# Optimization experiments

Hardware: AMD Instinct MI355X
Metric: run time of the kernel (lower is better)

Reference implementation:

```python
import jax, jax.numpy as jnp
import numpy as np

N_META, M_SUB = 64, 1024          # n meta-nodes, m nodes per sub-graph
D_IN, D_HID, D_OUT = 128, 128, 64
NUM_LAYERS_EXTRA, K = 2, 3        # total DSGraphGLayers = NUM_LAYERS_EXTRA + 1
N_EDGES = 1048576                 # ~avg degree 16 over 65536 nodes


def setup_inputs() -> dict:
    key = jax.random.key(0)
    ks = jax.random.split(key, 8)
    N = N_META * M_SUB
    x = jax.random.normal(ks[0], (N_META, M_SUB, D_IN), jnp.float32)
    sub_adj = jax.random.randint(ks[1], (2, N_EDGES), 0, N, dtype=jnp.int32)
    # dense binary meta-graph adjacency (n, n)
    adj = (jax.random.uniform(ks[2], (N_META, N_META)) < 0.1).astype(jnp.float32)
    L = NUM_LAYERS_EXTRA + 1
    scale = 1.0 / np.sqrt(D_HID).astype(np.float32)
    gcn_W = jax.random.normal(ks[3], (L, K + 1, D_HID, D_HID), jnp.float32) * scale
    gcn_b = jnp.zeros((L, K + 1, D_HID), jnp.float32)
    lin_W1 = jax.random.normal(ks[4], (D_HID, D_HID), jnp.float32) * scale
    lin_b1 = jnp.zeros((D_HID,), jnp.float32)
    lin_W2 = jax.random.normal(ks[5], (D_HID, D_OUT), jnp.float32) * scale
    lin_b2 = jnp.zeros((D_OUT,), jnp.float32)
    return dict(x=x, sub_adj=sub_adj, adj=adj, gcn_W=gcn_W, gcn_b=gcn_b,
                lin_W1=lin_W1, lin_b1=lin_b1, lin_W2=lin_W2, lin_b2=lin_b2)


def _gcn_conv(x, src, dst, dinv, W, b, N):
    norm = dinv[src] * dinv[dst]                      # [E+N]
    msg = (x @ W)[src] * norm[:, None]                # [E+N, d_out]
    return jax.ops.segment_sum(msg, dst, num_segments=N) + b


def reference(x, sub_adj, adj, gcn_W, gcn_b, lin_W1, lin_b1, lin_W2, lin_b2):
    n, m, d = x.shape
    N = n * m
    loops = jnp.arange(N, dtype=sub_adj.dtype)
    src = jnp.concatenate([sub_adj[0], loops])
    dst = jnp.concatenate([sub_adj[1], loops])
    deg = jax.ops.segment_sum(jnp.ones(src.shape, x.dtype), dst, num_segments=N)
    dinv = jnp.where(deg > 0, jax.lax.rsqrt(deg), jnp.zeros_like(deg))
    # precompute_adj: cached_adj = [adj, adj^2, ..., adj^K]; powers >= 2 detached in source
    cached = [adj]
    A = adj
    for _ in range(K - 1):
        A = jax.lax.stop_gradient(A @ adj)
        cached.append(A)
    for li in range(gcn_W.shape[0]):
        xf = x.reshape(N, -1)
        out = _gcn_conv(xf, src, dst, dinv, gcn_W[li, 0], gcn_b[li, 0], N)
        for i, Ai in enumerate(cached):
            # meta-graph mixing: x_i[n,m,d] = sum_j A_i[n,j] * x[j,m,d]
            xi = jnp.einsum('nj,jmd->nmd', Ai, x).reshape(N, -1)
            out = out + _gcn_conv(xi, src, dst, dinv, gcn_W[li, i + 1], gcn_b[li, i + 1], N)
        x = jax.nn.relu(out.reshape(n, m, -1))
    h = x.reshape(N, -1)
    h = jax.nn.relu(h @ lin_W1 + lin_b1)
    h = h @ lin_W2 + lin_b2
    return h.reshape(n, m, -1)
```

## Files before the change

### kernel.cpp

```cpp
#include <hip/hip_runtime.h>

#define NMETA 64
#define MSUB 1024
#define NNODES 65536
#define D 128
#define DOUT 64
#define NEDGES 1048576
#define COLS 131072
#define BCAP 5120

typedef __attribute__((ext_vector_type(8))) short bf8_t;
typedef __attribute__((ext_vector_type(4))) float f4_t;
typedef __attribute__((ext_vector_type(2))) float f2_t;

__device__ inline unsigned short bfr(float x) {
    unsigned u = __builtin_bit_cast(unsigned, x);
    u += 0x7fffu + ((u >> 16) & 1u);
    return (unsigned short)(u >> 16);
}
__device__ inline float b2f(unsigned short h) {
    return __builtin_bit_cast(float, (unsigned)h << 16);
}
__device__ inline f2_t up2(unsigned u) {
    f2_t r;
    r[0] = __builtin_bit_cast(float, u << 16);
    r[1] = __builtin_bit_cast(float, u & 0xffff0000u);
    return r;
}

__global__ __launch_bounds__(256) void k_bhist(const int* __restrict__ dst,
                                               int* __restrict__ whist) {
    __shared__ int c[256];
    int t = threadIdx.x, w = blockIdx.x;
    c[t] = 0;
    __syncthreads();
    const int* dp = dst + w * 4096;
    for (int k = 0; k < 16; ++k) atomicAdd(&c[dp[k * 256 + t] >> 8], 1);
    __syncthreads();
    whist[t * 256 + w] = c[t];
}

__global__ __launch_bounds__(256) void k_bscan(int* __restrict__ whist,
                                               int* __restrict__ bbase) {
    __shared__ int sh[256];
    int t = threadIdx.x;
    int run = 0;
    for (int w = 0; w < 256; ++w) {
        int v = whist[t * 256 + w];
        whist[t * 256 + w] = run;
        run += v;
    }
    sh[t] = run;
    __syncthreads();
    for (int d = 1; d < 256; d <<= 1) {
        int x = (t >= d) ? sh[t - d] : 0;
        __syncthreads();
        sh[t] += x;
        __syncthreads();
    }
    bbase[t] = sh[t] - run;
    if (t == 255) bbase[256] = NEDGES;
}

__global__ __launch_bounds__(256) void k_bscatter(const int* __restrict__ src,
                                                  const int* __restrict__ dst,
                                                  const int* __restrict__ bbase,
                                                  const int* __restrict__ whist,
                                                  unsigned* __restrict__ tmp) {
    __shared__ int cur[256];
    __shared__ int base[256];
    int t = threadIdx.x, w = blockIdx.x;
    cur[t] = 0;
    base[t] = bbase[t] + whist[t * 256 + w];
    __syncthreads();
    const int* dp = dst + w * 4096;
    const int* sp = src + w * 4096;
    for (int k = 0; k < 16; ++k) {
        int d = dp[k * 256 + t], s = sp[k * 256 + t];
        int b = d >> 8;
        int lr = atomicAdd(&cur[b], 1);
        tmp[base[b] + lr] = ((unsigned)(d & 255) << 16) | (unsigned)s;
    }
}

__global__ __launch_bounds__(256) void k_bcsr(const unsigned* __restrict__ tmp,
                                              const int* __restrict__ bbase,
                                              int* __restrict__ offs,
                                              float* __restrict__ dinv,
                                              unsigned short* __restrict__ csr16) {
    __shared__ unsigned pairs[BCAP];
    __shared__ unsigned short image[BCAP];
    __shared__ int cnt[256], cur[256], sh[256];
    int t = threadIdx.x, b = blockIdx.x;
    int base = bbase[b], n = bbase[b + 1] - base;
    for (int i = t; i < n; i += 256) pairs[i] = tmp[base + i];
    cnt[t] = 0;
    __syncthreads();
    for (int i = t; i < n; i += 256) atomicAdd(&cnt[pairs[i] >> 16], 1);
    __syncthreads();
    int c = cnt[t];
    sh[t] = c;
    __syncthreads();
    for (int d = 1; d < 256; d <<= 1) {
        int x = (t >= d) ? sh[t - d] : 0;
        __syncthreads();
        sh[t] += x;
        __syncthreads();
    }
    int excl = sh[t] - c;
    cur[t] = excl;
    offs[b * 256 + t] = base + excl;
    dinv[b * 256 + t] = rsqrtf((float)(c + 1));
    if (b == 255 && t == 255) offs[65536] = NEDGES;
    __syncthreads();
    for (int i = t; i < n; i += 256) {
        unsigned p = pairs[i];
        int pos = atomicAdd(&cur[p >> 16], 1);
        image[pos] = (unsigned short)(p & 0xffffu);
    }
    __syncthreads();
    {
        int s0 = excl, s1 = excl + c;
        for (int i = s0 + 1; i < s1; ++i) {
            unsigned short key = image[i];
            int j = i - 1;
            while (j >= s0 && image[j] > key) { image[j + 1] = image[j]; --j; }
            image[j + 1] = key;
        }
    }
    __syncthreads();
    for (int i = t; i < n; i += 256) csr16[base + i] = image[i];
}

__global__ __launch_bounds__(256) void k_setup(const float* __restrict__ A,
                                               unsigned short* __restrict__ Ab,
                                               const float* __restrict__ gcnW,
                                               const float* __restrict__ W1,
                                               const float* __restrict__ W2,
                                               unsigned short* __restrict__ Wt) {
    int blk = blockIdx.x, t = threadIdx.x;
    if (blk == 0) {
        __shared__ float As[4096];
        __shared__ float Bs[4096];
        for (int q = 0; q < 16; ++q) As[t + 256 * q] = A[t + 256 * q];
        __syncthreads();
        for (int q = 0; q < 16; ++q) {
            int idx = t + 256 * q;
            int n = idx >> 6, j = idx & 63;
            Ab[idx] = bfr(As[idx]);
            float acc = 0.f;
            for (int k = 0; k < 64; ++k) acc += As[n * 64 + k] * As[k * 64 + j];
            Bs[idx] = acc;
            Ab[4096 + idx] = bfr(acc);
        }
        __syncthreads();
        for (int q = 0; q < 16; ++q) {
            int idx = t + 256 * q;
            int n = idx >> 6, j = idx & 63;
            float acc = 0.f;
            for (int k = 0; k < 64; ++k) acc += Bs[n * 64 + k] * As[k * 64 + j];
            Ab[8192 + idx] = bfr(acc);
        }
    } else {
        int b2 = blk - 1;
        int m = b2 >> 6;
        int idx = (b2 & 63) * 256 + t;
        const float* src;
        int N = 128;
        if (m < 12)       src = gcnW + m * 16384;
        else if (m == 12) src = W1;
        else { src = W2; N = 64; if (idx >= 8192) return; }
        int n = idx >> 7, k = idx & 127;
        Wt[m * 16384 + idx] = bfr(src[k * N + n]);
    }
}

#define TS 130
template <bool INF32>
__global__ __launch_bounds__(256) void k_layer(const unsigned short* __restrict__ X,
                                               const float* __restrict__ Xf,
                                               const unsigned short* __restrict__ Ab,
                                               const unsigned short* __restrict__ Wt4,
                                               const float* __restrict__ dinv,
                                               unsigned short* __restrict__ Y) {
    __shared__ unsigned short LB[3 * 64 * TS];
    __shared__ float dsh[64];
    int t = threadIdx.x;
    int m = blockIdx.x;
    int wave = t >> 6, lane = t & 63;
    int l16 = lane & 15, kg = lane >> 4;
    int c0 = wave * 32;

    if (t < 64) dsh[t] = dinv[(long)t * MSUB + m];

#pragma unroll
    for (int it = 0; it < 4; ++it) {
        int slot = it * 256 + t;
        int row = slot >> 4, ch = slot & 15;
        if (INF32) {
            const float* xp = Xf + ((long)row * MSUB + m) * D + ch * 8;
            float4 va = *(const float4*)xp;
            float4 vb = *(const float4*)(xp + 4);
            uint4 pk;
            pk.x = ((unsigned)bfr(va.y) << 16) | bfr(va.x);
            pk.y = ((unsigned)bfr(va.w) << 16) | bfr(va.z);
            pk.z = ((unsigned)bfr(vb.y) << 16) | bfr(vb.x);
            pk.w = ((unsigned)bfr(vb.w) << 16) | bfr(vb.z);
            *(uint4*)&LB[row * 128 + ch * 8] = pk;
        } else {
            *(uint4*)&LB[row * 128 + ch * 8] =
                *(const uint4*)(X + ((long)row * MSUB + m) * D + ch * 8);
        }
    }
    __syncthreads();

    bf8_t xa[4][4];
#pragma unroll
    for (int mt = 0; mt < 4; ++mt)
#pragma unroll
        for (int kb = 0; kb < 4; ++kb)
            xa[mt][kb] = *(const bf8_t*)&LB[(mt * 16 + l16) * 128 + kb * 32 + kg * 8];
    __syncthreads();

    f4_t zero4 = {0.f, 0.f, 0.f, 0.f};

    f4_t accT0[4][2];
#pragma unroll
    for (int mt = 0; mt < 4; ++mt)
#pragma unroll
        for (int nt = 0; nt < 2; ++nt) accT0[mt][nt] = zero4;
#pragma unroll
    for (int kb = 0; kb < 4; ++kb)
#pragma unroll
        for (int nt = 0; nt < 2; ++nt) {
            bf8_t b = *(const bf8_t*)(Wt4 + (long)(c0 + nt * 16 + l16) * 128 +
                                      kb * 32 + kg * 8);
#pragma unroll
            for (int mt = 0; mt < 4; ++mt)
                accT0[mt][nt] = __builtin_amdgcn_mfma_f32_16x16x32_bf16(
                    xa[mt][kb], b, accT0[mt][nt], 0, 0, 0);
        }

#pragma unroll
    for (int z = 1; z < 4; ++z) {
        f4_t acc[4][2];
#pragma unroll
        for (int mt = 0; mt < 4; ++mt)
#pragma unroll
            for (int nt = 0; nt < 2; ++nt) acc[mt][nt] = zero4;
        const unsigned short* wp = Wt4 + z * 16384;
#pragma unroll
        for (int kb = 0; kb < 4; ++kb)
#pragma unroll
            for (int nt = 0; nt < 2; ++nt) {
                bf8_t b = *(const bf8_t*)(wp + (long)(c0 + nt * 16 + l16) * 128 +
                                          kb * 32 + kg * 8);
#pragma unroll
                for (int mt = 0; mt < 4; ++mt)
                    acc[mt][nt] = __builtin_amdgcn_mfma_f32_16x16x32_bf16(
                        xa[mt][kb], b, acc[mt][nt], 0, 0, 0);
            }
#pragma unroll
        for (int mt = 0; mt < 4; ++mt)
#pragma unroll
            for (int nt = 0; nt < 2; ++nt)
#pragma unroll
                for (int r = 0; r < 4; ++r)
                    LB[((z - 1) * 64 + mt * 16 + kg * 4 + r) * TS +
                       c0 + nt * 16 + l16] = bfr(acc[mt][nt][r]);
    }

    f4_t acc2[4][2];
#pragma unroll
    for (int mt = 0; mt < 4; ++mt)
#pragma unroll
        for (int nt = 0; nt < 2; ++nt) acc2[mt][nt] = zero4;
#pragma unroll
    for (int i = 0; i < 3; ++i)
#pragma unroll
        for (int kb = 0; kb < 2; ++kb) {
            bf8_t af[4];
#pragma unroll
            for (int mt = 0; mt < 4; ++mt)
                af[mt] = *(const bf8_t*)(Ab + i * 4096 + (mt * 16 + l16) * 64 +
                                         kb * 32 + kg * 8);
#pragma unroll
            for (int nt = 0; nt < 2; ++nt) {
                bf8_t b;
#pragma unroll
                for (int jj = 0; jj < 8; ++jj)
                    b[jj] = (short)LB[(i * 64 + kb * 32 + kg * 8 + jj) * TS +
                                      c0 + nt * 16 + l16];
#pragma unroll
                for (int mt = 0; mt < 4; ++mt)
                    acc2[mt][nt] = __builtin_amdgcn_mfma_f32_16x16x32_bf16(
                        af[mt], b, acc2[mt][nt], 0, 0, 0);
            }
        }

#pragma unroll
    for (int mt = 0; mt < 4; ++mt)
#pragma unroll
        for (int nt = 0; nt < 2; ++nt)
#pragma unroll
            for (int r = 0; r < 4; ++r) {
                int row = mt * 16 + kg * 4 + r;
                int col = c0 + nt * 16 + l16;
                float v = (acc2[mt][nt][r] + accT0[mt][nt][r]) * dsh[row];
                Y[((long)row * MSUB + m) * D + col] = bfr(v);
            }
}

__global__ __launch_bounds__(256) void k_prop(const unsigned short* __restrict__ Y,
                                              const int* __restrict__ offs,
                                              const unsigned short* __restrict__ csr,
                                              const float* __restrict__ dinv,
                                              const float* __restrict__ bias4,
                                              unsigned short* __restrict__ Xout) {
    int wid = threadIdx.x >> 6;
    int lane = threadIdx.x & 63;
    int q = lane >> 4;
    int l = lane & 15;
    int v = blockIdx.x * 4 + wid;
    const uint4* Y4 = (const uint4*)Y;
    int e0 = offs[v], e1 = offs[v + 1];
    f2_t acc2[4];
#pragma unroll
    for (int k = 0; k < 4; ++k) acc2[k] = (f2_t){0.f, 0.f};

    int e = e0 + q;
    for (; e + 4 < e1; e += 8) {
        int u0 = csr[e], u1 = csr[e + 4];
        uint4 y0 = Y4[(long)u0 * 16 + l];
        uint4 y1 = Y4[(long)u1 * 16 + l];
        acc2[0] += up2(y0.x) + up2(y1.x);
        acc2[1] += up2(y0.y) + up2(y1.y);
        acc2[2] += up2(y0.z) + up2(y1.z);
        acc2[3] += up2(y0.w) + up2(y1.w);
    }
    if (e < e1) {
        int u = csr[e];
        uint4 y = Y4[(long)u * 16 + l];
        acc2[0] += up2(y.x);
        acc2[1] += up2(y.y);
        acc2[2] += up2(y.z);
        acc2[3] += up2(y.w);
    }
    float acc[8];
#pragma unroll
    for (int k = 0; k < 4; ++k) { acc[2 * k] = acc2[k][0]; acc[2 * k + 1] = acc2[k][1]; }
#pragma unroll
    for (int k = 0; k < 8; ++k) {
        acc[k] += __shfl_xor(acc[k], 32, 64);
        acc[k] += __shfl_xor(acc[k], 16, 64);
    }
    if (q == 0) {
        float dv = dinv[v];
        uint4 s = Y4[(long)v * 16 + l];
        f2_t s2[4] = {up2(s.x), up2(s.y), up2(s.z), up2(s.w)};
        float bs[8];
#pragma unroll
        for (int k = 0; k < 8; ++k) bs[k] = 0.f;
#pragma unroll
        for (int p = 0; p < 4; ++p) {
            float4 blo = *(const float4*)(bias4 + p * 128 + l * 8);
            float4 bhi = *(const float4*)(bias4 + p * 128 + l * 8 + 4);
            bs[0] += blo.x; bs[1] += blo.y; bs[2] += blo.z; bs[3] += blo.w;
            bs[4] += bhi.x; bs[5] += bhi.y; bs[6] += bhi.z; bs[7] += bhi.w;
        }
        unsigned r[8];
#pragma unroll
        for (int k = 0; k < 8; ++k) {
            float sf = s2[k / 2][k % 2];
            r[k] = bfr(fmaxf(dv * (acc[k] + sf) + bs[k], 0.f));
        }
        uint4 pk;
        pk.x = (r[1] << 16) | r[0];
        pk.y = (r[3] << 16) | r[2];
        pk.z = (r[5] << 16) | r[4];
        pk.w = (r[7] << 16) | r[6];
        ((uint4*)Xout)[(long)v * 16 + l] = pk;
    }
}

#define HST 136
__global__ __launch_bounds__(256) void k_mlp(const unsigned short* __restrict__ X,
                                             const unsigned short* __restrict__ Wt,
                                             const float* __restrict__ b1,
                                             const float* __restrict__ b2,
                                             float* __restrict__ out) {
    __shared__ unsigned short H[128 * HST];
    int wave = threadIdx.x >> 6, lane = threadIdx.x & 63;
    int l16 = lane & 15, kg = lane >> 4;
    long row0 = (long)blockIdx.x * 128 + wave * 32;
    int hb = wave * 32 * HST;

    bf8_t a[2][4];
    const unsigned short* xp = X + row0 * 128 + kg * 8;
#pragma unroll
    for (int kb = 0; kb < 4; ++kb) {
        a[0][kb] = *(const bf8_t*)(xp + (long)l16 * 128 + kb * 32);
        a[1][kb] = *(const bf8_t*)(xp + (long)(l16 + 16) * 128 + kb * 32);
    }
    f4_t zero4 = {0.f, 0.f, 0.f, 0.f};
    f4_t acc[2][8];
#pragma unroll
    for (int mt = 0; mt < 2; ++mt)
#pragma unroll
        for (int nt = 0; nt < 8; ++nt) acc[mt][nt] = zero4;

    const unsigned short* wp = Wt + 12 * 16384 + (long)l16 * 128 + kg * 8;
#pragma unroll
    for (int kb = 0; kb < 4; ++kb)
#pragma unroll
        for (int nt = 0; nt < 8; ++nt) {
            bf8_t b = *(const bf8_t*)(wp + nt * 16 * 128 + kb * 32);
            acc[0][nt] = __builtin_amdgcn_mfma_f32_16x16x32_bf16(a[0][kb], b, acc[0][nt], 0, 0, 0);
            acc[1][nt] = __builtin_amdgcn_mfma_f32_16x16x32_bf16(a[1][kb], b, acc[1][nt], 0, 0, 0);
        }

#pragma unroll
    for (int nt = 0; nt < 8; ++nt) {
        float bv = b1[nt * 16 + l16];
#pragma unroll
        for (int mt = 0; mt < 2; ++mt)
#pragma unroll
            for (int r = 0; r < 4; ++r) {
                int row = mt * 16 + kg * 4 + r;
                H[hb + row * HST + nt * 16 + l16] = bfr(fmaxf(acc[mt][nt][r] + bv, 0.f));
            }
    }

    bf8_t h2[2][4];
#pragma unroll
    for (int kb = 0; kb < 4; ++kb) {
        h2[0][kb] = *(const bf8_t*)&H[hb + l16 * HST + kb * 32 + kg * 8];
        h2[1][kb] = *(const bf8_t*)&H[hb + (l16 + 16) * HST + kb * 32 + kg * 8];
    }
    f4_t acc2[2][4];
#pragma unroll
    for (int mt = 0; mt < 2; ++mt)
#pragma unroll
        for (int nt = 0; nt < 4; ++nt) acc2[mt][nt] = zero4;
    const unsigned short* w2 = Wt + 13 * 16384 + (long)l16 * 128 + kg * 8;
#pragma unroll
    for (int kb = 0; kb < 4; ++kb)
#pragma unroll
        for (int nt = 0; nt < 4; ++nt) {
            bf8_t b = *(const bf8_t*)(w2 + nt * 16 * 128 + kb * 32);
            acc2[0][nt] = __builtin_amdgcn_mfma_f32_16x16x32_bf16(h2[0][kb], b, acc2[0][nt], 0, 0, 0);
            acc2[1][nt] = __builtin_amdgcn_mfma_f32_16x16x32_bf16(h2[1][kb], b, acc2[1][nt], 0, 0, 0);
        }
#pragma unroll
    for (int mt = 0; mt < 2; ++mt)
#pragma unroll
        for (int nt = 0; nt < 4; ++nt)
#pragma unroll
            for (int r = 0; r < 4; ++r) {
                long row = row0 + mt * 16 + kg * 4 + r;
                int col = nt * 16 + l16;
                out[row * DOUT + col] = acc2[mt][nt][r] + b2[col];
            }
}

extern "C" void kernel_launch(void* const* d_in, const int* in_sizes, int n_in,
                              void* d_out, int out_size, void* d_ws, size_t ws_size,
                              hipStream_t stream) {
    const float* x      = (const float*)d_in[0];
    const int*   subadj = (const int*)d_in[1];
    const float* adj    = (const float*)d_in[2];
    const float* gcn_W  = (const float*)d_in[3];
    const float* gcn_b  = (const float*)d_in[4];
    const float* lin_W1 = (const float*)d_in[5];
    const float* lin_b1 = (const float*)d_in[6];
    const float* lin_W2 = (const float*)d_in[7];
    const float* lin_b2 = (const float*)d_in[8];
    float* out = (float*)d_out;

    const int* e_src = subadj;
    const int* e_dst = subadj + NEDGES;

    char* w = (char*)d_ws;
    int*      whist = (int*)w;      w += (size_t)65536 * 4;
    int*      bbase = (int*)w;      w += (size_t)260 * 4;
    int*      offs  = (int*)w;      w += (size_t)65540 * 4;
    float*    dinv  = (float*)w;    w += (size_t)65536 * 4;
    unsigned* tmp   = (unsigned*)w; w += (size_t)NEDGES * 4;
    unsigned short* csr16 = (unsigned short*)w; w += (size_t)NEDGES * 2;
    unsigned short* Ab  = (unsigned short*)w; w += (size_t)3 * 4096 * 2;
    unsigned short* Xbf = (unsigned short*)w; w += (size_t)NNODES * D * 2;
    unsigned short* Ybf = (unsigned short*)w; w += (size_t)NNODES * D * 2;
    unsigned short* Wt  = (unsigned short*)w; w += (size_t)14 * 16384 * 2;

    k_bhist<<<256, 256, 0, stream>>>(e_dst, whist);
    k_bscan<<<1, 256, 0, stream>>>(whist, bbase);
    k_bscatter<<<256, 256, 0, stream>>>(e_src, e_dst, bbase, whist, tmp);
    k_bcsr<<<256, 256, 0, stream>>>(tmp, bbase, offs, dinv, csr16);
    k_setup<<<897, 256, 0, stream>>>(adj, Ab, gcn_W, lin_W1, lin_W2, Wt);

    for (int li = 0; li < 3; ++li) {
        if (li == 0)
            k_layer<true><<<MSUB, 256, 0, stream>>>(nullptr, x, Ab, Wt, dinv, Ybf);
        else
            k_layer<false><<<MSUB, 256, 0, stream>>>(Xbf, nullptr, Ab,
                                                     Wt + (size_t)li * 4 * 16384, dinv, Ybf);
        k_prop<<<NNODES / 4, 256, 0, stream>>>(Ybf, offs, csr16, dinv,
                                               gcn_b + (size_t)li * 512, Xbf);
    }
    k_mlp<<<NNODES / 128, 256, 0, stream>>>(Xbf, Wt, lin_b1, lin_b2, out);
}
```

Before: 502.9 us.

## Use per-wave swizzled transposed LDS slab and fuse meta-mixing into z loop

The k_layer kernel now stores each intermediate X·W_z tile transposed into a per-wave, XOR-swizzled LDS slab using packed 64-bit writes. The meta-mixing MFMA reads its B operand as one 128-bit load instead of eight scalar strided loads. The mixing for each z is done right after its GEMM and accumulates straight into the T0 accumulator, which removes the separate accumulator and cuts LDS from a 3x64x130 buffer to 8192 shorts. This is meant to reduce LDS instruction count and bank conflicts, raise occupancy, and lower register pressure, but it depends on each wave's slab being private, since no barrier separates successive z iterations.

```diff
diff --git a/kernel.cpp b/kernel.cpp
--- a/kernel.cpp
+++ b/kernel.cpp
@@ -12,6 +12,7 @@
 typedef __attribute__((ext_vector_type(8))) short bf8_t;
 typedef __attribute__((ext_vector_type(4))) float f4_t;
 typedef __attribute__((ext_vector_type(2))) float f2_t;
+typedef __attribute__((ext_vector_type(2))) unsigned ui2_t;
 
 __device__ inline unsigned short bfr(float x) {
     unsigned u = __builtin_bit_cast(unsigned, x);
@@ -175,7 +176,6 @@
     }
 }
 
-#define TS 130
 template <bool INF32>
 __global__ __launch_bounds__(256) void k_layer(const unsigned short* __restrict__ X,
                                                const float* __restrict__ Xf,
@@ -183,7 +183,7 @@
                                                const unsigned short* __restrict__ Wt4,
                                                const float* __restrict__ dinv,
                                                unsigned short* __restrict__ Y) {
-    __shared__ unsigned short LB[3 * 64 * TS];
+    __shared__ unsigned short LB[8192];
     __shared__ float dsh[64];
     int t = threadIdx.x;
     int m = blockIdx.x;
@@ -224,11 +224,11 @@
 
     f4_t zero4 = {0.f, 0.f, 0.f, 0.f};
 
-    f4_t accT0[4][2];
+    f4_t acc2[4][2];
 #pragma unroll
     for (int mt = 0; mt < 4; ++mt)
 #pragma unroll
-        for (int nt = 0; nt < 2; ++nt) accT0[mt][nt] = zero4;
+        for (int nt = 0; nt < 2; ++nt) acc2[mt][nt] = zero4;
 #pragma unroll
     for (int kb = 0; kb < 4; ++kb)
 #pragma unroll
@@ -237,10 +237,12 @@
                                       kb * 32 + kg * 8);
 #pragma unroll
             for (int mt = 0; mt < 4; ++mt)
-                accT0[mt][nt] = __builtin_amdgcn_mfma_f32_16x16x32_bf16(
-                    xa[mt][kb], b, accT0[mt][nt], 0, 0, 0);
-        }
-
+                acc2[mt][nt] = __builtin_amdgcn_mfma_f32_16x16x32_bf16(
+                    xa[mt][kb], b, acc2[mt][nt], 0, 0, 0);
+        }
+
+    char* slab = (char*)&LB[wave * 2048];
+    const unsigned swz = (unsigned)((l16 & 7) << 4);
 #pragma unroll
     for (int z = 1; z < 4; ++z) {
         f4_t acc[4][2];
@@ -263,20 +265,17 @@
 #pragma unroll
         for (int mt = 0; mt < 4; ++mt)
 #pragma unroll
-            for (int nt = 0; nt < 2; ++nt)
-#pragma unroll
-                for (int r = 0; r < 4; ++r)
-                    LB[((z - 1) * 64 + mt * 16 + kg * 4 + r) * TS +
-                       c0 + nt * 16 + l16] = bfr(acc[mt][nt][r]);
-    }
-
-    f4_t acc2[4][2];
-#pragma unroll
-    for (int mt = 0; mt < 4; ++mt)
-#pragma unroll
-        for (int nt = 0; nt < 2; ++nt) acc2[mt][nt] = zero4;
-#pragma unroll
-    for (int i = 0; i < 3; ++i)
+            for (int nt = 0; nt < 2; ++nt) {
+                unsigned lo = (unsigned)bfr(acc[mt][nt][0]) |
+                              ((unsigned)bfr(acc[mt][nt][1]) << 16);
+                unsigned hi = (unsigned)bfr(acc[mt][nt][2]) |
+                              ((unsigned)bfr(acc[mt][nt][3]) << 16);
+                ui2_t pk = {lo, hi};
+                unsigned boff =
+                    (unsigned)(((nt * 16 + l16) * 64 + mt * 16 + kg * 4) * 2) ^ swz;
+                *(ui2_t*)(slab + boff) = pk;
+            }
+        int i = z - 1;
 #pragma unroll
         for (int kb = 0; kb < 2; ++kb) {
             bf8_t af[4];
@@ -286,17 +285,16 @@
                                          kb * 32 + kg * 8);
 #pragma unroll
             for (int nt = 0; nt < 2; ++nt) {
-                bf8_t b;
-#pragma unroll
-                for (int jj = 0; jj < 8; ++jj)
-                    b[jj] = (short)LB[(i * 64 + kb * 32 + kg * 8 + jj) * TS +
-                                      c0 + nt * 16 + l16];
+                unsigned boff =
+                    (unsigned)(((nt * 16 + l16) * 64 + kb * 32 + kg * 8) * 2) ^ swz;
+                bf8_t b = *(const bf8_t*)(slab + boff);
 #pragma unroll
                 for (int mt = 0; mt < 4; ++mt)
                     acc2[mt][nt] = __builtin_amdgcn_mfma_f32_16x16x32_bf16(
                         af[mt], b, acc2[mt][nt], 0, 0, 0);
             }
         }
+    }
 
 #pragma unroll
     for (int mt = 0; mt < 4; ++mt)
@@ -306,7 +304,7 @@
             for (int r = 0; r < 4; ++r) {
                 int row = mt * 16 + kg * 4 + r;
                 int col = c0 + nt * 16 + l16;
-                float v = (acc2[mt][nt][r] + accT0[mt][nt][r]) * dsh[row];
+                float v = acc2[mt][nt][r] * dsh[row];
                 Y[((long)row * MSUB + m) * D + col] = bfr(v);
             }
 }
```

Result: faster. 483.6 us (-3.8%).
